# Kernel tuning notes

Hardware: AMD Instinct MI355X
Metric: run time of the kernel (lower is better)

## Reference

```python
import jax, jax.numpy as jnp
import numpy as np

WINDOW = 10


def setup_inputs() -> dict:
    key = jax.random.key(0)
    k_r, k_w1, k_b1, k_w2, k_b2 = jax.random.split(key, 5)
    B, T = 2048, 4096
    returns = jax.random.normal(k_r, (B, T), dtype=jnp.float32)
    # nn.Linear default init ~ U(-1/sqrt(fan_in), 1/sqrt(fan_in)); scaled normals are fine for a reference
    W1 = jax.random.normal(k_w1, (32, WINDOW), dtype=jnp.float32) / np.sqrt(WINDOW)
    b1 = jax.random.normal(k_b1, (32,), dtype=jnp.float32) * 0.01
    W2 = jax.random.normal(k_w2, (1, 32), dtype=jnp.float32) / np.sqrt(32)
    b2 = jax.random.normal(k_b2, (1,), dtype=jnp.float32) * 0.01
    return {"returns": returns, "W1": W1, "b1": b1, "W2": W2, "b2": b2}


def reference(returns, W1, b1, W2, b2) -> jnp.ndarray:
    B, T = returns.shape
    w = WINDOW
    # Gather all sliding windows at once: window i covers returns[:, i:i+w] and
    # produces the estimate for timestep t = i + w (matching the torch loop).
    idx = jnp.arange(T - w)[:, None] + jnp.arange(w)[None, :]  # [T-w, w]
    wins = returns[:, idx]  # [B, T-w, w]
    h1 = jax.nn.relu(jnp.einsum('btw,hw->bth', wins, W1) + b1)  # [B, T-w, 32]
    h = 0.5 * jax.nn.sigmoid(jnp.einsum('bth,oh->bto', h1, W2) + b2)[..., 0]  # [B, T-w]
    # H[:, :window] = H[:, window] (the first computed value)
    head = jnp.broadcast_to(h[:, :1], (B, w))
    return jnp.concatenate([head, h], axis=1)  # [B, T]
```

## Files before the change

### kernel.cpp

```cpp
#include <hip/hip_runtime.h>

#define WINDOW 10
#define TDIM 4096
#define TVALID (TDIM - WINDOW)

typedef __attribute__((ext_vector_type(8)))  short bf16x8;
typedef __attribute__((ext_vector_type(8)))  __bf16 bfv8;
typedef __attribute__((ext_vector_type(8)))  float f32x8;
typedef __attribute__((ext_vector_type(16))) float f32x16;
typedef __attribute__((ext_vector_type(2)))  float f32x2;
typedef float f32x4u __attribute__((ext_vector_type(4), aligned(4)));

static __device__ __forceinline__ short f2bf(float f) {
  return (short)__builtin_bit_cast(unsigned short, (__bf16)f);
}

static __device__ __forceinline__ float l2dot(const f32x16& acc, const f32x2* __restrict__ w2p) {
  f32x2 s0 = {0.f, 0.f}, s1 = {0.f, 0.f};
  #pragma unroll
  for (int j = 0; j < 8; j += 2) {
    f32x2 a, b;
    a[0] = fmaxf(acc[2*j],     0.f); a[1] = fmaxf(acc[2*j + 1], 0.f);
    b[0] = fmaxf(acc[2*j + 2], 0.f); b[1] = fmaxf(acc[2*j + 3], 0.f);
    s0 = __builtin_elementwise_fma(a, w2p[j],     s0);
    s1 = __builtin_elementwise_fma(b, w2p[j + 1], s1);
  }
  f32x2 s = s0 + s1;
  return s[0] + s[1];
}

static __device__ __forceinline__ float combine_halves(float Pe, float Po, int lid) {
#if __has_builtin(__builtin_amdgcn_permlane32_swap)
  auto r = __builtin_amdgcn_permlane32_swap(
      __builtin_bit_cast(unsigned, Pe), __builtin_bit_cast(unsigned, Po), false, false);
  return __builtin_bit_cast(float, (unsigned)r[0]) + __builtin_bit_cast(float, (unsigned)r[1]);
#else
  Pe += __shfl_xor(Pe, 32, 64);
  Po += __shfl_xor(Po, 32, 64);
  return (lid < 32) ? Pe : Po;
#endif
}

static __device__ __forceinline__ float half_sigmoid(float z) {
  float e = __expf(-z);
#if __has_builtin(__builtin_amdgcn_rcpf)
  return 0.5f * __builtin_amdgcn_rcpf(1.0f + e);
#else
  return 0.5f / (1.0f + e);
#endif
}

struct Setup {
  bf16x8 af; f32x2 w2p[8]; float b2c;
  int lid, n, g; bool g1;
};
static __device__ __forceinline__ Setup make_setup(
    const float* __restrict__ W1, const float* __restrict__ b1,
    const float* __restrict__ W2, const float* __restrict__ b2) {
  Setup s;
  s.lid = threadIdx.x & 63; s.n = s.lid & 31; s.g = s.lid >> 5; s.g1 = (s.g == 1);
  if (!s.g1) {
    #pragma unroll
    for (int j = 0; j < 8; ++j) s.af[j] = f2bf(W1[s.n * WINDOW + j]);
  } else {
    s.af[0] = f2bf(W1[s.n * WINDOW + 8]);
    s.af[1] = f2bf(W1[s.n * WINDOW + 9]);
    s.af[2] = f2bf(b1[s.n]);
    #pragma unroll
    for (int j = 3; j < 8; ++j) s.af[j] = 0;
  }
  #pragma unroll
  for (int j = 0; j < 8; ++j) {
    s.w2p[j][0] = W2[((2*j)   & 3) + 8 * ((2*j)   >> 2) + 4 * s.g];
    s.w2p[j][1] = W2[((2*j+1) & 3) + 8 * ((2*j+1) >> 2) + 4 * s.g];
  }
  s.b2c = b2[0];
  return s;
}

static __device__ __forceinline__ f32x8 ld8(const float* __restrict__ p) {
  f32x4u a = *(const f32x4u*)p;
  f32x4u b = *(const f32x4u*)(p + 4);
  f32x8 f; f[0]=a[0];f[1]=a[1];f[2]=a[2];f[3]=a[3];f[4]=b[0];f[5]=b[1];f[6]=b[2];f[7]=b[3];
  return f;
}
static __device__ __forceinline__ bf16x8 packbf(f32x8 f, bool g1) {
  f[2] = g1 ? 1.0f : f[2];
  return __builtin_bit_cast(bf16x8, __builtin_convertvector(f, bfv8));
}

static __device__ __forceinline__ float pair_f32(
    const Setup& S, const float* __restrict__ rowp, int seg, int p, bool clamp) {
  const int lbase = S.n + 8 * S.g;
  f32x8 fe = ld8(rowp + seg + p * 64 + lbase);
  f32x8 fo;
  if (clamp) {
    for (int j = 0; j < 8; ++j) {
      int idx = seg + p * 64 + 32 + lbase + j;
      idx = idx < TDIM - 1 ? idx : TDIM - 1;
      fo[j] = rowp[idx];
    }
  } else {
    fo = ld8(rowp + seg + p * 64 + 32 + lbase);
  }
  bf16x8 bve = packbf(fe, S.g1), bvo = packbf(fo, S.g1);
  f32x16 acce = {}, acco = {};
  acce = __builtin_amdgcn_mfma_f32_32x32x16_bf16(S.af, bve, acce, 0, 0, 0);
  acco = __builtin_amdgcn_mfma_f32_32x32x16_bf16(S.af, bvo, acco, 0, 0, 0);
  float Pe = l2dot(acce, S.w2p);
  float Po = l2dot(acco, S.w2p);
  const float q = combine_halves(Pe, Po, S.lid);
  return half_sigmoid(q + S.b2c);
}

__global__ __launch_bounds__(256) void hurst_tlp(
    const float* __restrict__ ret, const float* __restrict__ W1,
    const float* __restrict__ b1,  const float* __restrict__ W2,
    const float* __restrict__ b2,  float* __restrict__ out) {
  Setup S = make_setup(W1, b1, W2, b2);
  const int wv    = threadIdx.x >> 6;
  const int row   = blockIdx.x;
  const int chunk = blockIdx.y;
  const int seg   = chunk * 1024 + wv * 256;

  const float* __restrict__ rowp = ret + (size_t)row * TDIM;
  float* __restrict__ orow = out + (size_t)row * TDIM;

  float y = pair_f32(S, rowp, seg, 0, false);
  orow[WINDOW + seg + S.lid] = y;
  if (chunk == 0 && wv == 0) {
    const float y0 = __shfl(y, 0, 64);
    if (S.lid < WINDOW) orow[S.lid] = y0;
  }
  #pragma unroll
  for (int p = 1; p < 3; ++p) {
    y = pair_f32(S, rowp, seg, p, false);
    orow[WINDOW + seg + p * 64 + S.lid] = y;
  }
  const bool tail = (chunk == 3) && (wv == 3);
  y = pair_f32(S, rowp, seg, 3, tail);
  const int t = seg + 3 * 64 + S.lid;
  if (!tail || t < TVALID) orow[WINDOW + t] = y;
}

extern "C" void kernel_launch(void* const* d_in, const int* in_sizes, int n_in,
                              void* d_out, int out_size, void* d_ws, size_t ws_size,
                              hipStream_t stream) {
  const float* ret = (const float*)d_in[0];
  const float* W1  = (const float*)d_in[1];
  const float* b1  = (const float*)d_in[2];
  const float* W2  = (const float*)d_in[3];
  const float* b2  = (const float*)d_in[4];
  float* out = (float*)d_out;

  const int B = in_sizes[0] / TDIM;
  dim3 block(256);
  dim3 grid(B, 4);
  hipLaunchKernelGGL(hurst_tlp, grid, block, 0, stream,
                     ret, W1, b1, W2, b2, out);
}
```

Measured before the change: 47.05 us.

## Stage whole input row in LDS and process one row per block

```diff
diff --git a/kernel.cpp b/kernel.cpp
--- a/kernel.cpp
+++ b/kernel.cpp
@@ -3,6 +3,7 @@
 #define WINDOW 10
 #define TDIM 4096
 #define TVALID (TDIM - WINDOW)
+#define LROW 4160
 
 typedef __attribute__((ext_vector_type(8)))  short bf16x8;
 typedef __attribute__((ext_vector_type(8)))  __bf16 bfv8;
@@ -10,6 +11,7 @@
 typedef __attribute__((ext_vector_type(16))) float f32x16;
 typedef __attribute__((ext_vector_type(2)))  float f32x2;
 typedef float f32x4u __attribute__((ext_vector_type(4), aligned(4)));
+typedef float f32x4a __attribute__((ext_vector_type(4), aligned(16)));
 
 static __device__ __forceinline__ short f2bf(float f) {
   return (short)__builtin_bit_cast(unsigned short, (__bf16)f);
@@ -78,31 +80,23 @@
   return s;
 }
 
-static __device__ __forceinline__ f32x8 ld8(const float* __restrict__ p) {
-  f32x4u a = *(const f32x4u*)p;
-  f32x4u b = *(const f32x4u*)(p + 4);
-  f32x8 f; f[0]=a[0];f[1]=a[1];f[2]=a[2];f[3]=a[3];f[4]=b[0];f[5]=b[1];f[6]=b[2];f[7]=b[3];
-  return f;
-}
 static __device__ __forceinline__ bf16x8 packbf(f32x8 f, bool g1) {
   f[2] = g1 ? 1.0f : f[2];
   return __builtin_bit_cast(bf16x8, __builtin_convertvector(f, bfv8));
 }
 
-static __device__ __forceinline__ float pair_f32(
-    const Setup& S, const float* __restrict__ rowp, int seg, int p, bool clamp) {
-  const int lbase = S.n + 8 * S.g;
-  f32x8 fe = ld8(rowp + seg + p * 64 + lbase);
-  f32x8 fo;
-  if (clamp) {
-    for (int j = 0; j < 8; ++j) {
-      int idx = seg + p * 64 + 32 + lbase + j;
-      idx = idx < TDIM - 1 ? idx : TDIM - 1;
-      fo[j] = rowp[idx];
-    }
-  } else {
-    fo = ld8(rowp + seg + p * 64 + 32 + lbase);
-  }
+static __device__ __forceinline__ f32x8 lds_ld8(const float* __restrict__ p) {
+  f32x8 f;
+  #pragma unroll
+  for (int j = 0; j < 8; ++j) f[j] = p[j];
+  return f;
+}
+
+static __device__ __forceinline__ float pair_lds(
+    const Setup& S, const float* __restrict__ srow, int seg, int p) {
+  const float* base = srow + seg + p * 64 + S.n + 8 * S.g;
+  f32x8 fe = lds_ld8(base);
+  f32x8 fo = lds_ld8(base + 32);
   bf16x8 bve = packbf(fe, S.g1), bvo = packbf(fo, S.g1);
   f32x16 acce = {}, acco = {};
   acce = __builtin_amdgcn_mfma_f32_32x32x16_bf16(S.af, bve, acce, 0, 0, 0);
@@ -113,34 +107,61 @@
   return half_sigmoid(q + S.b2c);
 }
 
-__global__ __launch_bounds__(256) void hurst_tlp(
+__global__ __launch_bounds__(256) void hurst_lds(
     const float* __restrict__ ret, const float* __restrict__ W1,
     const float* __restrict__ b1,  const float* __restrict__ W2,
     const float* __restrict__ b2,  float* __restrict__ out) {
-  Setup S = make_setup(W1, b1, W2, b2);
-  const int wv    = threadIdx.x >> 6;
-  const int row   = blockIdx.x;
-  const int chunk = blockIdx.y;
-  const int seg   = chunk * 1024 + wv * 256;
+  __shared__ float srow[LROW];
 
+  const int row = blockIdx.x;
   const float* __restrict__ rowp = ret + (size_t)row * TDIM;
   float* __restrict__ orow = out + (size_t)row * TDIM;
 
-  float y = pair_f32(S, rowp, seg, 0, false);
+  {
+    const int tid = threadIdx.x;
+    #pragma unroll
+    for (int it = 0; it < 3; ++it) {
+      const int c = tid + it * 256;
+      if (c < LROW / 8) {
+        f32x8 f;
+        if (c < TDIM / 8) {
+          f32x4u a = *(const f32x4u*)(rowp + 8 * c);
+          f32x4u b = *(const f32x4u*)(rowp + 8 * c + 4);
+          f[0]=a[0]; f[1]=a[1]; f[2]=a[2]; f[3]=a[3];
+          f[4]=b[0]; f[5]=b[1]; f[6]=b[2]; f[7]=b[3];
+        } else {
+          const float last = rowp[TDIM - 1];
+          #pragma unroll
+          for (int j = 0; j < 8; ++j) f[j] = last;
+        }
+        f32x4a lo = {f[0], f[1], f[2], f[3]};
+        f32x4a hi = {f[4], f[5], f[6], f[7]};
+        *(f32x4a*)(srow + 8 * c)     = lo;
+        *(f32x4a*)(srow + 8 * c + 4) = hi;
+      }
+    }
+  }
+
+  Setup S = make_setup(W1, b1, W2, b2);
+  __syncthreads();
+
+  const int wv  = threadIdx.x >> 6;
+  const int seg = wv * 1024;
+
+  float y = pair_lds(S, srow, seg, 0);
   orow[WINDOW + seg + S.lid] = y;
-  if (chunk == 0 && wv == 0) {
+  if (wv == 0) {
     const float y0 = __shfl(y, 0, 64);
     if (S.lid < WINDOW) orow[S.lid] = y0;
   }
   #pragma unroll
-  for (int p = 1; p < 3; ++p) {
-    y = pair_f32(S, rowp, seg, p, false);
+  for (int p = 1; p < 15; ++p) {
+    y = pair_lds(S, srow, seg, p);
     orow[WINDOW + seg + p * 64 + S.lid] = y;
   }
-  const bool tail = (chunk == 3) && (wv == 3);
-  y = pair_f32(S, rowp, seg, 3, tail);
-  const int t = seg + 3 * 64 + S.lid;
-  if (!tail || t < TVALID) orow[WINDOW + t] = y;
+  y = pair_lds(S, srow, seg, 15);
+  const int t = seg + 15 * 64 + S.lid;
+  if (t < TVALID) orow[WINDOW + t] = y;
 }
 
 extern "C" void kernel_launch(void* const* d_in, const int* in_sizes, int n_in,
@@ -155,7 +176,7 @@
 
   const int B = in_sizes[0] / TDIM;
   dim3 block(256);
-  dim3 grid(B, 4);
-  hipLaunchKernelGGL(hurst_tlp, grid, block, 0, stream,
+  dim3 grid(B);
+  hipLaunchKernelGGL(hurst_lds, grid, block, 0, stream,
                      ret, W1, b1, W2, b2, out);
 }
```

New measurement: 44.09 us. 1.07x faster.
